# Optimization experiments

Hardware: AMD Instinct MI355X
Metric: run time of the kernel (lower is better)

Reference implementation:

```python
import jax, jax.numpy as jnp
import numpy as np

EPS = 1e-5

def _conv(x, w, b):
    # NCHW, OIHW, stride 1, SAME padding (kernel 3, padding 1)
    y = jax.lax.conv_general_dilated(x, w, (1, 1), 'SAME',
                                     dimension_numbers=('NCHW', 'OIHW', 'NCHW'))
    return y + b[None, :, None, None]

def _maxpool2(x):
    return jax.lax.reduce_window(x, -jnp.inf, jax.lax.max,
                                 (1, 1, 2, 2), (1, 1, 2, 2), 'VALID')

def _fraud_layer(v, theta, phases, sq_r, disp_r, disp_phi, kerr):
    # classical shim of a 2-mode photonic layer; all params are zero -> identity
    c, s = jnp.cos(theta), jnp.sin(theta)
    rot = jnp.array([[1.0, 0.0], [0.0, 1.0]]) * c + jnp.array([[0.0, -1.0], [1.0, 0.0]]) * s
    v = v @ rot.T
    v = v * jnp.cos(phases)          # phase shifters
    v = v * jnp.exp(sq_r)            # squeezing
    v = v + disp_r * jnp.cos(disp_phi)  # displacement
    return v + kerr * v ** 3         # Kerr nonlinearity

def setup_inputs() -> dict:
    key = jax.random.key(0)
    ks = jax.random.split(key, 16)
    B = 4096
    inp = {
        'x': jax.random.normal(ks[0], (B, 1, 32, 32), jnp.float32),
        'conv1_w': jax.random.normal(ks[1], (8, 1, 3, 3), jnp.float32) * 0.2,
        'conv1_b': jnp.zeros((8,), jnp.float32),
        'conv2_w': jax.random.normal(ks[2], (16, 8, 3, 3), jnp.float32) * 0.1,
        'conv2_b': jnp.zeros((16,), jnp.float32),
        'conv3_w': jax.random.normal(ks[3], (32, 16, 3, 3), jnp.float32) * 0.1,
        'conv3_b': jnp.zeros((32,), jnp.float32),
        'gnn_w1': jax.random.normal(ks[4], (32, 32), jnp.float32) * 0.2,
        'gnn_w2': jax.random.normal(ks[5], (16, 32), jnp.float32) * 0.2,
        'rotation_params': jax.random.normal(ks[6], (4, 4), jnp.float32),
        'entangle_params': jax.random.normal(ks[7], (3,), jnp.float32),
        'reduce_w': jax.random.normal(ks[8], (2, 32), jnp.float32) * 0.2,
        'reduce_b': jnp.zeros((2,), jnp.float32),
        'cls_w': jax.random.normal(ks[9], (2, 2), jnp.float32) * 0.5,
        'cls_b': jnp.zeros((2,), jnp.float32),
        'bn_gamma': jnp.ones((2,), jnp.float32),
        'bn_beta': jnp.zeros((2,), jnp.float32),
    }
    return inp

def reference(x, conv1_w, conv1_b, conv2_w, conv2_b, conv3_w, conv3_b,
              gnn_w1, gnn_w2, rotation_params, entangle_params,
              reduce_w, reduce_b, cls_w, cls_b, bn_gamma, bn_beta):
    B = x.shape[0]
    # CNN feature extractor
    h = jax.nn.relu(_conv(x, conv1_w, conv1_b))
    h = _maxpool2(h)
    h = jax.nn.relu(_conv(h, conv2_w, conv2_b))
    h = _maxpool2(h)
    h = jax.nn.relu(_conv(h, conv3_w, conv3_b))
    feats = jnp.mean(h, axis=(2, 3))  # AdaptiveAvgPool2d((1,1)) -> (B, 32)
    # GNN feedforward (batched equivalent of the per-sample Python loop)
    a = jnp.tanh(feats @ gnn_w1.T)    # (B, 32)
    g = jnp.tanh(a @ gnn_w2.T)        # (B, 16)
    # Quantum-style self-attention (runs on detached numpy in original -> stop_gradient)
    d = g.shape[-1]
    q = (g.reshape(B, 4, 4) @ rotation_params).reshape(B, d)
    k = (g.reshape(B, 4, 4) @ rotation_params.T).reshape(B, d)
    temp = jnp.mean(jnp.cos(entangle_params))
    logits = (q @ k.T) * (temp / jnp.sqrt(jnp.asarray(d, jnp.float32)))  # (B, B)
    attn = jax.nn.softmax(logits, axis=-1) @ g                           # (B, 16)
    rep = jnp.concatenate([g, attn], axis=-1)                            # (B, 32)
    rep = jax.lax.stop_gradient(rep)  # numpy round-trip breaks the autograd graph
    # reduce -> fraud layers (all-zero params -> identity) -> classifier
    reduced = rep @ reduce_w.T + reduce_b  # (B, 2)
    z = jnp.zeros((2,), jnp.float32)
    for _ in range(2):  # input layer + 1 hidden layer, all-zero FraudLayerParameters
        reduced = _fraud_layer(reduced, 0.0, z, z, z, z, z)
    out = reduced @ cls_w.T + cls_b  # (B, 2)
    # BatchNorm1d(2) in training mode: batch stats, biased variance
    mu = jnp.mean(out, axis=0)
    var = jnp.mean((out - mu) ** 2, axis=0)
    out = bn_gamma * (out - mu) * jax.lax.rsqrt(var + EPS) + bn_beta
    return out
```

## Files before the change

### kernel.cpp

```cpp
#include <hip/hip_runtime.h>
#include <math.h>

#define LOG2E 1.4426950408889634f

typedef _Float16 h2v __attribute__((ext_vector_type(2)));
typedef _Float16 h4  __attribute__((ext_vector_type(4)));
typedef _Float16 h8  __attribute__((ext_vector_type(8)));
typedef float    f4  __attribute__((ext_vector_type(4)));

__device__ __forceinline__ h2v pk(float a, float b) {
    return __builtin_bit_cast(h2v, __builtin_amdgcn_cvt_pkrtz(a, b));
}

__device__ __forceinline__ f4 mfma16x32(h8 a, h8 b, f4 c) {
    return __builtin_amdgcn_mfma_f32_16x16x32_f16(a, b, c, 0, 0, 0);
}

__device__ __forceinline__ f4 mfma16x16(h4 a, h4 b, f4 c) {
    return __builtin_amdgcn_mfma_f32_16x16x16f16(a, b, c, 0, 0, 0);
}

__device__ __forceinline__ float fast_tanh(float x) {
    const float xc = fminf(fmaxf(x, -15.f), 15.f);
    const float t = exp2f(xc * (2.f * LOG2E));
    return (t - 1.f) * __builtin_amdgcn_rcpf(t + 1.f);
}

__global__ __launch_bounds__(256) void k_pack(
    const float* __restrict__ w1,
    const float* __restrict__ w2, const float* __restrict__ w3,
    const float* __restrict__ ent,
    _Float16* __restrict__ w2f, _Float16* __restrict__ w3f,
    h2v* __restrict__ w1p, float* __restrict__ w1t,
    float* __restrict__ tsc)
{
    if (threadIdx.x == 0) {
        const float temp = (cosf(ent[0]) + cosf(ent[1]) + cosf(ent[2])) * (1.f / 3.f);
        tsc[0] = temp * 0.25f;
    }
    if (threadIdx.x < 24) {
        const int oc = threadIdx.x / 3, ky = threadIdx.x % 3;
        w1p[threadIdx.x] = pk(w1[oc * 9 + ky * 3 + 0], w1[oc * 9 + ky * 3 + 1]);
        w1t[threadIdx.x] = w1[oc * 9 + ky * 3 + 2];
    }
    for (int idx = threadIdx.x; idx < 1536; idx += 256) {
        const int j = idx & 7;
        const int lane = (idx >> 3) & 63;
        const int c = idx >> 9;
        const int oc = lane & 15;
        const int s = c * 4 + (lane >> 4);
        w2f[idx] = (s < 9) ? (_Float16)w2[oc * 72 + j * 9 + s] : (_Float16)0.f;
    }
    for (int idx = threadIdx.x; idx < 5120; idx += 256) {
        const int j = idx & 7;
        const int lane = (idx >> 3) & 63;
        const int rest = idx >> 9;
        const int mt = rest / 5;
        const int oc = mt * 16 + (lane & 15);
        const int kk = (lane >> 4) * 8 + j;
        const int ic = kk & 15;
        const int sh = (rest - mt * 5) * 2 + (kk >> 4);
        w3f[idx] = (sh < 9) ? (_Float16)w3[oc * 144 + ic * 9 + sh] : (_Float16)0.f;
    }
}

__global__ __launch_bounds__(256) void k_cnn(
    const float* __restrict__ x,
    const h2v* __restrict__ w1p, const float* __restrict__ w1t,
    const float* __restrict__ b1,
    const _Float16* __restrict__ w2f, const float* __restrict__ b2,
    const _Float16* __restrict__ w3f, const float* __restrict__ b3,
    const float* __restrict__ gw1,
    const float* __restrict__ gw2,
    const float* __restrict__ rot,
    const float* __restrict__ tsc,
    _Float16* __restrict__ q16, _Float16* __restrict__ k16,
    _Float16* __restrict__ g16, _Float16* __restrict__ gswz)
{
    __shared__ __align__(16) char smem[4624 + 5184 + 3200 + 256];
    float* xs   = (float*)smem;
    h8*  p1c    = (h8*)(smem + 4624);
    h8*  p2hc   = (h8*)(smem + 4624 + 5184);
    h4*  p2h4   = (h4*)(smem + 4624 + 5184);
    float* fsum = (float*)(smem + 4624 + 5184 + 3200);

    const int t = threadIdx.x;
    const int b = blockIdx.x;
    const int lane = t & 63;
    const int w = __builtin_amdgcn_readfirstlane(t >> 6);
    const int nn = lane & 15;
    const int kq = lane >> 4;

    const h8 hzero = (h8)(_Float16)0.f;
    const f4 fzero = {0.f, 0.f, 0.f, 0.f};

    const float4 v = ((const float4*)(x + (size_t)b * 1024))[t];

    if (t < 132) {
        int r, c;
        if (t < 34)       { r = 0;  c = t; }
        else if (t < 68)  { r = 33; c = t - 34; }
        else if (t < 100) { r = t - 68 + 1;  c = 0; }
        else              { r = t - 100 + 1; c = 33; }
        xs[r * 34 + c] = 0.f;
    } else if (t < 200) {
        const int u = t - 132;
        int r, c;
        if (u < 18)      { r = 0;  c = u; }
        else if (u < 36) { r = 17; c = u - 18; }
        else if (u < 52) { r = u - 36 + 1; c = 0; }
        else             { r = u - 52 + 1; c = 17; }
        p1c[r * 18 + c] = hzero;
    } else if (t < 236) {
        const int u = t - 200;
        int r, c;
        if (u < 10)      { r = 0; c = u; }
        else if (u < 20) { r = 9; c = u - 10; }
        else if (u < 28) { r = u - 20 + 1; c = 0; }
        else             { r = u - 28 + 1; c = 9; }
        p2hc[(r * 10 + c) * 2 + 0] = hzero;
        p2hc[(r * 10 + c) * 2 + 1] = hzero;
    }
    {
        const int row = t >> 3;
        const int col = (t & 7) << 2;
        float* dst = &xs[(row + 1) * 34 + col + 1];
        dst[0] = v.x; dst[1] = v.y; dst[2] = v.z; dst[3] = v.w;
    }
    __syncthreads();

    {
        const int px = t & 15, py = t >> 4;
        float pa[4][4];
        #pragma unroll
        for (int iy = 0; iy < 4; ++iy)
            #pragma unroll
            for (int ix = 0; ix < 4; ++ix)
                pa[iy][ix] = xs[(2 * py + iy) * 34 + (2 * px + ix)];
        h2v pA[4], pB[4];
        #pragma unroll
        for (int r = 0; r < 4; ++r) {
            pA[r] = pk(pa[r][0], pa[r][1]);
            pB[r] = pk(pa[r][1], pa[r][2]);
        }

        float r8[8];
        #pragma unroll
        for (int oc = 0; oc < 8; ++oc) {
            const h2v wp0 = w1p[oc * 3 + 0], wp1 = w1p[oc * 3 + 1], wp2 = w1p[oc * 3 + 2];
            const float wt0 = w1t[oc * 3 + 0], wt1 = w1t[oc * 3 + 1], wt2 = w1t[oc * 3 + 2];
            const float bb = b1[oc];
            float mx = -1e30f;
            #pragma unroll
            for (int sy = 0; sy < 2; ++sy) {
                float s0 = bb, s1 = bb;
                s0 = __builtin_amdgcn_fdot2(pA[sy],     wp0, s0, false);
                s0 = __builtin_amdgcn_fdot2(pA[sy + 1], wp1, s0, false);
                s0 = __builtin_amdgcn_fdot2(pA[sy + 2], wp2, s0, false);
                s0 = fmaf(pa[sy][2], wt0, s0);
                s0 = fmaf(pa[sy + 1][2], wt1, s0);
                s0 = fmaf(pa[sy + 2][2], wt2, s0);
                s1 = __builtin_amdgcn_fdot2(pB[sy],     wp0, s1, false);
                s1 = __builtin_amdgcn_fdot2(pB[sy + 1], wp1, s1, false);
                s1 = __builtin_amdgcn_fdot2(pB[sy + 2], wp2, s1, false);
                s1 = fmaf(pa[sy][3], wt0, s1);
                s1 = fmaf(pa[sy + 1][3], wt1, s1);
                s1 = fmaf(pa[sy + 2][3], wt2, s1);
                mx = fmaxf(mx, fmaxf(s0, s1));
            }
            r8[oc] = fmaxf(mx, 0.f);
        }
        union { h8 v; h2v p[4]; } u;
        #pragma unroll
        for (int ocp = 0; ocp < 4; ++ocp) u.p[ocp] = pk(r8[2 * ocp], r8[2 * ocp + 1]);
        p1c[(py + 1) * 18 + (px + 1)] = u.v;
    }

    h8 a2[3];
    #pragma unroll
    for (int c = 0; c < 3; ++c) a2[c] = ((const h8*)w2f)[c * 64 + lane];

    __syncthreads();

    f4 accp[4] = {fzero, fzero, fzero, fzero};
    #pragma unroll
    for (int c = 0; c < 3; ++c) {
        const int s = c * 4 + kq;
        const int ky = (s < 9) ? s / 3 : 0;
        const int kx = (s < 9) ? s % 3 : 0;
        #pragma unroll
        for (int p = 0; p < 4; ++p) {
            h8 bf = hzero;
            if (s < 9) bf = p1c[(4 * w + p + ky) * 18 + (nn + kx)];
            accp[p] = mfma16x32(a2[c], bf, accp[p]);
        }
    }

    {
        float bq[4];
        #pragma unroll
        for (int r = 0; r < 4; ++r) bq[r] = b2[kq * 4 + r];
        #pragma unroll
        for (int i = 0; i < 2; ++i) {
            float m2[4];
            #pragma unroll
            for (int r = 0; r < 4; ++r) {
                const float v0 = fmaxf(accp[2 * i][r] + bq[r], 0.f);
                const float v1 = fmaxf(accp[2 * i + 1][r] + bq[r], 0.f);
                float mv = fmaxf(v0, v1);
                mv = fmaxf(mv, __shfl_xor(mv, 1));
                m2[r] = mv;
            }
            if ((lane & 1) == 0) {
                const int px = nn >> 1;
                const int py = 2 * w + i;
                union { h4 v; h2v p[2]; } u;
                u.p[0] = pk(m2[0], m2[1]);
                u.p[1] = pk(m2[2], m2[3]);
                p2h4[((py + 1) * 10 + (px + 1)) * 4 + kq] = u.v;
            }
        }
    }

    const int mt = w >> 1;
    const int nt0 = (w & 1) * 2;
    h8 a3[5];
    #pragma unroll
    for (int c = 0; c < 5; ++c) a3[c] = ((const h8*)w3f)[(mt * 5 + c) * 64 + lane];

    __syncthreads();

    f4 acc3[2] = {fzero, fzero};
    #pragma unroll
    for (int c = 0; c < 5; ++c) {
        const int shv = 2 * c + (kq >> 1);
        const int hh = kq & 1;
        const int ky = (shv < 9) ? ((shv * 11) >> 5) : 0;
        const int kx = (shv < 9) ? (shv - 3 * ky) : 0;
        #pragma unroll
        for (int p = 0; p < 2; ++p) {
            const int pos = (nt0 + p) * 16 + nn;
            const int yy = pos >> 3, xx = pos & 7;
            h8 bf = hzero;
            if (shv < 9) bf = p2hc[((yy + ky) * 10 + (xx + kx)) * 2 + hh];
            acc3[p] = mfma16x32(a3[c], bf, acc3[p]);
        }
    }

    {
        float bq[4];
        #pragma unroll
        for (int r = 0; r < 4; ++r) bq[r] = b3[mt * 16 + kq * 4 + r];
        float sv[4];
        #pragma unroll
        for (int r = 0; r < 4; ++r) {
            float s = fmaxf(acc3[0][r] + bq[r], 0.f) + fmaxf(acc3[1][r] + bq[r], 0.f);
            #pragma unroll
            for (int off = 1; off < 16; off <<= 1) s += __shfl_xor(s, off);
            sv[r] = s;
        }
        if (nn == 0) {
            const f4 pack = {sv[0], sv[1], sv[2], sv[3]};
            ((f4*)fsum)[mt * 8 + (w & 1) * 4 + kq] = pack;
        }
    }
    __syncthreads();

    if (w != 0) return;

    const float qscale = tsc[0];

    const int l = t;
    const int i5 = l & 31;
    const float fsv = (fsum[(i5 >> 4) * 32 + (i5 & 15)] +
                       fsum[(i5 >> 4) * 32 + 16 + (i5 & 15)]) * (1.f / 64.f);

    float asv;
    {
        const int h = l >> 5;
        float s = 0.f;
        #pragma unroll
        for (int q4 = 0; q4 < 4; ++q4) {
            const float4 wv = ((const float4*)gw1)[i5 * 8 + h * 4 + q4];
            s = fmaf(wv.x, __shfl(fsv, h * 16 + q4 * 4 + 0), s);
            s = fmaf(wv.y, __shfl(fsv, h * 16 + q4 * 4 + 1), s);
            s = fmaf(wv.z, __shfl(fsv, h * 16 + q4 * 4 + 2), s);
            s = fmaf(wv.w, __shfl(fsv, h * 16 + q4 * 4 + 3), s);
        }
        s += __shfl_xor(s, 32);
        asv = fast_tanh(s);
    }

    const int i4 = l & 15;
    float gsv;
    {
        const int h = l >> 4;
        float s = 0.f;
        #pragma unroll
        for (int q4 = 0; q4 < 2; ++q4) {
            const float4 wv = ((const float4*)gw2)[i4 * 8 + h * 2 + q4];
            s = fmaf(wv.x, __shfl(asv, h * 8 + q4 * 4 + 0), s);
            s = fmaf(wv.y, __shfl(asv, h * 8 + q4 * 4 + 1), s);
            s = fmaf(wv.z, __shfl(asv, h * 8 + q4 * 4 + 2), s);
            s = fmaf(wv.w, __shfl(asv, h * 8 + q4 * 4 + 3), s);
        }
        s += __shfl_xor(s, 16);
        s += __shfl_xor(s, 32);
        gsv = fast_tanh(s);
    }

    const int grp = l >> 4;
    const int r = i4 >> 2, c = i4 & 3;
    float gq[4];
    #pragma unroll
    for (int j = 0; j < 4; ++j) gq[j] = __shfl(gsv, r * 4 + j);

    float v2;
    if (grp == 0) {
        v2 = 0.f;
        #pragma unroll
        for (int j = 0; j < 4; ++j) v2 = fmaf(gq[j], rot[j * 4 + c], v2);
        v2 *= qscale;
    } else if (grp == 1) {
        v2 = 0.f;
        #pragma unroll
        for (int j = 0; j < 4; ++j) v2 = fmaf(gq[j], rot[c * 4 + j], v2);
    } else {
        v2 = gsv;
    }
    const float vn = __shfl_xor(v2, 1);

    if (grp == 3) {
        const int tile = b >> 4, lc = b & 15;
        gswz[tile * 256 + (((lc >> 2) * 16) + i4) * 4 + (lc & 3)] = (_Float16)gsv;
    } else if ((i4 & 1) == 0) {
        const h2v pv = pk(v2, vn);
        if (grp == 0)      ((h2v*)q16)[b * 8 + (i4 >> 1)] = pv;
        else if (grp == 1) ((h2v*)k16)[b * 8 + (i4 >> 1)] = pv;
        else               ((h2v*)g16)[b * 8 + (i4 >> 1)] = pv;
    }
}

__global__ __launch_bounds__(1024) void k_attn(
    const _Float16* __restrict__ q16, const _Float16* __restrict__ k16,
    const _Float16* __restrict__ g16, const _Float16* __restrict__ gswz,
    const float* __restrict__ rw, const float* __restrict__ rb,
    const float* __restrict__ cw, const float* __restrict__ cb,
    float* __restrict__ outp, int B)
{
    __shared__ f4 lO[16][64];
    __shared__ float lm[16][16];
    __shared__ float ll[16][16];

    const int t = threadIdx.x;
    const int lane = t & 63;
    const int w = t >> 6;
    const int rt = blockIdx.x;
    const int r = lane & 15;
    const int q = lane >> 4;
    const f4 fzero = {0.f, 0.f, 0.f, 0.f};

    const h4 qf = *(const h4*)(q16 + ((size_t)(rt * 16 + r)) * 16 + q * 4);

    float m = -1e30f, lp = 0.f;
    f4 O = fzero;

    const int strip = B >> 4;
    const int cbeg = w * strip;

    h4 kf = *(const h4*)(k16 + ((size_t)(cbeg + r)) * 16 + q * 4);
    h4 gf = *(const h4*)(gswz + (size_t)(cbeg >> 4) * 256 + lane * 4);

    for (int ci = 0; ci < strip; ci += 16) {
        const int cnext = (ci + 16 < strip) ? (cbeg + ci + 16) : cbeg;
        const h4 kf_n = *(const h4*)(k16 + ((size_t)(cnext + r)) * 16 + q * 4);
        const h4 gf_n = *(const h4*)(gswz + (size_t)(cnext >> 4) * 256 + lane * 4);

        const f4 st = mfma16x16(kf, qf, fzero);

        float mx = fmaxf(fmaxf(st[0], st[1]), fmaxf(st[2], st[3]));
        mx = fmaxf(mx, __shfl_xor(mx, 16));
        mx = fmaxf(mx, __shfl_xor(mx, 32));
        if (__ballot(mx > m)) {
            const float mn = fmaxf(m, mx);
            const float a = exp2f((m - mn) * LOG2E);
            lp *= a;
            O[0] *= a; O[1] *= a; O[2] *= a; O[3] *= a;
            m = mn;
        }
        const float p0 = exp2f((st[0] - m) * LOG2E);
        const float p1 = exp2f((st[1] - m) * LOG2E);
        const float p2 = exp2f((st[2] - m) * LOG2E);
        const float p3 = exp2f((st[3] - m) * LOG2E);
        lp += (p0 + p1) + (p2 + p3);

        union { h4 v; h2v p[2]; } u;
        u.p[0] = pk(p0, p1);
        u.p[1] = pk(p2, p3);
        O = mfma16x16(gf, u.v, O);

        kf = kf_n;
        gf = gf_n;
    }
    lp += __shfl_xor(lp, 16);
    lp += __shfl_xor(lp, 32);

    lO[w][lane] = O;
    if (lane < 16) { lm[w][lane] = m; ll[w][lane] = lp; }
    __syncthreads();

    if (w == 0) {
        float M = lm[0][r];
        #pragma unroll
        for (int ww = 1; ww < 16; ++ww) M = fmaxf(M, lm[ww][r]);
        float L = 0.f;
        f4 Om = fzero;
        #pragma unroll
        for (int ww = 0; ww < 16; ++ww) {
            const float f = exp2f((lm[ww][r] - M) * LOG2E);
            L = fmaf(ll[ww][r], f, L);
            const f4 ow = lO[ww][lane];
            Om[0] = fmaf(ow[0], f, Om[0]);
            Om[1] = fmaf(ow[1], f, Om[1]);
            Om[2] = fmaf(ow[2], f, Om[2]);
            Om[3] = fmaf(ow[3], f, Om[3]);
        }
        const float il = 1.f / L;
        const h4 gr = *(const h4*)(g16 + ((size_t)(rt * 16 + r)) * 16 + q * 4);

        float rv[2];
        #pragma unroll
        for (int c = 0; c < 2; ++c) {
            float s = 0.f;
            #pragma unroll
            for (int j = 0; j < 4; ++j) {
                s = fmaf((float)gr[j], rw[c * 32 + q * 4 + j], s);
                s = fmaf(Om[j] * il, rw[c * 32 + 16 + q * 4 + j], s);
            }
            s += __shfl_xor(s, 16);
            s += __shfl_xor(s, 32);
            rv[c] = s + rb[c];
        }
        if (q == 0) {
            float2 o;
            o.x = cb[0] + cw[0] * rv[0] + cw[1] * rv[1];
            o.y = cb[1] + cw[2] * rv[0] + cw[3] * rv[1];
            ((float2*)outp)[rt * 16 + r] = o;
        }
    }
}

__global__ __launch_bounds__(1024) void k_bn(
    float* __restrict__ data, const float* __restrict__ gamma,
    const float* __restrict__ beta, int B)
{
    __shared__ float red[16][4];
    __shared__ float coef[4];
    const int t = threadIdx.x;
    float s0 = 0.f, s1 = 0.f, q0 = 0.f, q1 = 0.f;
    for (int i = t; i < B; i += 1024) {
        const float2 v = ((const float2*)data)[i];
        s0 += v.x; q0 += v.x * v.x;
        s1 += v.y; q1 += v.y * v.y;
    }
    #pragma unroll
    for (int off = 32; off; off >>= 1) {
        s0 += __shfl_xor(s0, off); q0 += __shfl_xor(q0, off);
        s1 += __shfl_xor(s1, off); q1 += __shfl_xor(q1, off);
    }
    if ((t & 63) == 0) {
        red[t >> 6][0] = s0; red[t >> 6][1] = q0;
        red[t >> 6][2] = s1; red[t >> 6][3] = q1;
    }
    __syncthreads();
    if (t == 0) {
        float S0 = 0.f, Q0 = 0.f, S1 = 0.f, Q1 = 0.f;
        for (int w = 0; w < 16; ++w) {
            S0 += red[w][0]; Q0 += red[w][1]; S1 += red[w][2]; Q1 += red[w][3];
        }
        const float inv = 1.f / (float)B;
        const float mu0 = S0 * inv, mu1 = S1 * inv;
        const float v0 = Q0 * inv - mu0 * mu0;
        const float v1 = Q1 * inv - mu1 * mu1;
        const float sc0 = gamma[0] * rsqrtf(v0 + 1e-5f);
        const float sc1 = gamma[1] * rsqrtf(v1 + 1e-5f);
        coef[0] = sc0; coef[1] = beta[0] - mu0 * sc0;
        coef[2] = sc1; coef[3] = beta[1] - mu1 * sc1;
    }
    __syncthreads();
    const float sc0 = coef[0], sh0 = coef[1], sc1 = coef[2], sh1 = coef[3];
    for (int i = t; i < B; i += 1024) {
        float2 v = ((const float2*)data)[i];
        v.x = fmaf(v.x, sc0, sh0);
        v.y = fmaf(v.y, sc1, sh1);
        ((float2*)data)[i] = v;
    }
}

extern "C" void kernel_launch(void* const* d_in, const int* in_sizes, int n_in,
                              void* d_out, int out_size, void* d_ws, size_t ws_size,
                              hipStream_t stream)
{
    (void)n_in; (void)out_size; (void)ws_size;
    const float* x   = (const float*)d_in[0];
    const float* w1  = (const float*)d_in[1];
    const float* b1  = (const float*)d_in[2];
    const float* w2  = (const float*)d_in[3];
    const float* b2  = (const float*)d_in[4];
    const float* w3  = (const float*)d_in[5];
    const float* b3  = (const float*)d_in[6];
    const float* gw1 = (const float*)d_in[7];
    const float* gw2 = (const float*)d_in[8];
    const float* rot = (const float*)d_in[9];
    const float* ent = (const float*)d_in[10];
    const float* rw  = (const float*)d_in[11];
    const float* rbv = (const float*)d_in[12];
    const float* cw  = (const float*)d_in[13];
    const float* cbv = (const float*)d_in[14];
    const float* gam = (const float*)d_in[15];
    const float* bet = (const float*)d_in[16];

    const int B = in_sizes[0] / (32 * 32);

    _Float16* q16  = (_Float16*)d_ws;
    _Float16* k16  = q16 + (size_t)B * 16;
    _Float16* g16  = k16 + (size_t)B * 16;
    _Float16* gswz = g16 + (size_t)B * 16;
    _Float16* w2f  = gswz + (size_t)B * 16;
    _Float16* w3f  = w2f + 1536;
    h2v*      w1p  = (h2v*)(w3f + 5120);
    float*    w1t  = (float*)(w1p + 24);
    float*    tsc  = w1t + 24;
    float* pre = (float*)d_out;

    k_pack<<<1, 256, 0, stream>>>(w1, w2, w3, ent, w2f, w3f, w1p, w1t, tsc);
    k_cnn<<<B, 256, 0, stream>>>(x, w1p, w1t, b1, w2f, b2, w3f, b3, gw1, gw2,
                                 rot, tsc, q16, k16, g16, gswz);
    k_attn<<<B / 16, 1024, 0, stream>>>(q16, k16, g16, gswz, rw, rbv, cw, cbv,
                                        pre, B);
    k_bn<<<1, 1024, 0, stream>>>(pre, gam, bet, B);
}
```

Before: 133.8 us.

## Use MFMA for conv1, deepen attention prefetch, fuse BN stats via atomics

Conv1 plus maxpool is recast as a 32x32x16 MFMA. A packed weight matrix covers the four pool sub-positions times eight output channels, and the 4x4 input patch is the K dimension. The attention loop prefetches two key/value tiles ahead instead of one. BatchNorm sums and squared sums are accumulated with atomics inside the attention kernel, so the BN kernel no longer rereads and reduces the whole output. In exchange, conv1 inputs are rounded to fp16, the atomic float sums are nondeterministic, and register pressure rises from the deeper prefetch.

```diff
diff --git a/kernel.cpp b/kernel.cpp
--- a/kernel.cpp
+++ b/kernel.cpp
@@ -7,6 +7,7 @@
 typedef _Float16 h4  __attribute__((ext_vector_type(4)));
 typedef _Float16 h8  __attribute__((ext_vector_type(8)));
 typedef float    f4  __attribute__((ext_vector_type(4)));
+typedef float    f16v __attribute__((ext_vector_type(16)));
 
 __device__ __forceinline__ h2v pk(float a, float b) {
     return __builtin_bit_cast(h2v, __builtin_amdgcn_cvt_pkrtz(a, b));
@@ -14,6 +15,10 @@
 
 __device__ __forceinline__ f4 mfma16x32(h8 a, h8 b, f4 c) {
     return __builtin_amdgcn_mfma_f32_16x16x32_f16(a, b, c, 0, 0, 0);
+}
+
+__device__ __forceinline__ f16v mfma32x16(h8 a, h8 b, f16v c) {
+    return __builtin_amdgcn_mfma_f32_32x32x16_f16(a, b, c, 0, 0, 0);
 }
 
 __device__ __forceinline__ f4 mfma16x16(h4 a, h4 b, f4 c) {
@@ -31,17 +36,24 @@
     const float* __restrict__ w2, const float* __restrict__ w3,
     const float* __restrict__ ent,
     _Float16* __restrict__ w2f, _Float16* __restrict__ w3f,
-    h2v* __restrict__ w1p, float* __restrict__ w1t,
-    float* __restrict__ tsc)
+    _Float16* __restrict__ w1a, float* __restrict__ tsc,
+    float* __restrict__ bnacc)
 {
     if (threadIdx.x == 0) {
         const float temp = (cosf(ent[0]) + cosf(ent[1]) + cosf(ent[2])) * (1.f / 3.f);
         tsc[0] = temp * 0.25f;
     }
-    if (threadIdx.x < 24) {
-        const int oc = threadIdx.x / 3, ky = threadIdx.x % 3;
-        w1p[threadIdx.x] = pk(w1[oc * 9 + ky * 3 + 0], w1[oc * 9 + ky * 3 + 1]);
-        w1t[threadIdx.x] = w1[oc * 9 + ky * 3 + 2];
+    if (threadIdx.x < 4) bnacc[threadIdx.x] = 0.f;
+    for (int idx = threadIdx.x; idx < 512; idx += 256) {
+        const int ln = idx >> 3, j = idx & 7;
+        const int m = ln & 31;
+        const int k = ((ln >> 5) << 3) + j;
+        const int sidx = m >> 3, oc = m & 7;
+        const int sy = sidx >> 1, sx = sidx & 1;
+        const int ry = (k >> 2) - sy, rx = (k & 3) - sx;
+        float val = 0.f;
+        if (ry >= 0 && ry < 3 && rx >= 0 && rx < 3) val = w1[oc * 9 + ry * 3 + rx];
+        w1a[idx] = (_Float16)val;
     }
     for (int idx = threadIdx.x; idx < 1536; idx += 256) {
         const int j = idx & 7;
@@ -66,7 +78,7 @@
 
 __global__ __launch_bounds__(256) void k_cnn(
     const float* __restrict__ x,
-    const h2v* __restrict__ w1p, const float* __restrict__ w1t,
+    const _Float16* __restrict__ w1a,
     const float* __restrict__ b1,
     const _Float16* __restrict__ w2f, const float* __restrict__ b2,
     const _Float16* __restrict__ w3f, const float* __restrict__ b3,
@@ -95,6 +107,8 @@
     const f4 fzero = {0.f, 0.f, 0.f, 0.f};
 
     const float4 v = ((const float4*)(x + (size_t)b * 1024))[t];
+    const h8 a1 = ((const h8*)w1a)[lane];
+    const float4 bb4 = ((const float4*)b1)[lane >> 5];
 
     if (t < 132) {
         int r, c;
@@ -130,50 +144,31 @@
     __syncthreads();
 
     {
-        const int px = t & 15, py = t >> 4;
-        float pa[4][4];
-        #pragma unroll
-        for (int iy = 0; iy < 4; ++iy)
-            #pragma unroll
-            for (int ix = 0; ix < 4; ++ix)
-                pa[iy][ix] = xs[(2 * py + iy) * 34 + (2 * px + ix)];
-        h2v pA[4], pB[4];
-        #pragma unroll
-        for (int r = 0; r < 4; ++r) {
-            pA[r] = pk(pa[r][0], pa[r][1]);
-            pB[r] = pk(pa[r][1], pa[r][2]);
-        }
-
-        float r8[8];
-        #pragma unroll
-        for (int oc = 0; oc < 8; ++oc) {
-            const h2v wp0 = w1p[oc * 3 + 0], wp1 = w1p[oc * 3 + 1], wp2 = w1p[oc * 3 + 2];
-            const float wt0 = w1t[oc * 3 + 0], wt1 = w1t[oc * 3 + 1], wt2 = w1t[oc * 3 + 2];
-            const float bb = b1[oc];
-            float mx = -1e30f;
-            #pragma unroll
-            for (int sy = 0; sy < 2; ++sy) {
-                float s0 = bb, s1 = bb;
-                s0 = __builtin_amdgcn_fdot2(pA[sy],     wp0, s0, false);
-                s0 = __builtin_amdgcn_fdot2(pA[sy + 1], wp1, s0, false);
-                s0 = __builtin_amdgcn_fdot2(pA[sy + 2], wp2, s0, false);
-                s0 = fmaf(pa[sy][2], wt0, s0);
-                s0 = fmaf(pa[sy + 1][2], wt1, s0);
-                s0 = fmaf(pa[sy + 2][2], wt2, s0);
-                s1 = __builtin_amdgcn_fdot2(pB[sy],     wp0, s1, false);
-                s1 = __builtin_amdgcn_fdot2(pB[sy + 1], wp1, s1, false);
-                s1 = __builtin_amdgcn_fdot2(pB[sy + 2], wp2, s1, false);
-                s1 = fmaf(pa[sy][3], wt0, s1);
-                s1 = fmaf(pa[sy + 1][3], wt1, s1);
-                s1 = fmaf(pa[sy + 2][3], wt2, s1);
-                mx = fmaxf(mx, fmaxf(s0, s1));
-            }
-            r8[oc] = fmaxf(mx, 0.f);
-        }
-        union { h8 v; h2v p[4]; } u;
-        #pragma unroll
-        for (int ocp = 0; ocp < 4; ++ocp) u.p[ocp] = pk(r8[2 * ocp], r8[2 * ocp + 1]);
-        p1c[(py + 1) * 18 + (px + 1)] = u.v;
+        const int n = lane & 31, h = lane >> 5;
+        const float2* xs2 = (const float2*)xs;
+        const f16v z16 = (f16v)0.f;
+        #pragma unroll
+        for (int sub = 0; sub < 2; ++sub) {
+            const int p = w * 64 + sub * 32 + n;
+            const int pyy = p >> 4, pxx = p & 15;
+            const int base = (2 * pyy + 2 * h) * 17 + pxx;
+            const float2 v00 = xs2[base],      v01 = xs2[base + 1];
+            const float2 v10 = xs2[base + 17], v11 = xs2[base + 18];
+            union { h8 v; h2v p2[4]; } bu;
+            bu.p2[0] = pk(v00.x, v00.y);
+            bu.p2[1] = pk(v01.x, v01.y);
+            bu.p2[2] = pk(v10.x, v10.y);
+            bu.p2[3] = pk(v11.x, v11.y);
+            const f16v acc = mfma32x16(a1, bu.v, z16);
+            float o0 = fmaxf(fmaxf(fmaxf(acc[0], acc[4]),  fmaxf(acc[8],  acc[12])) + bb4.x, 0.f);
+            float o1 = fmaxf(fmaxf(fmaxf(acc[1], acc[5]),  fmaxf(acc[9],  acc[13])) + bb4.y, 0.f);
+            float o2 = fmaxf(fmaxf(fmaxf(acc[2], acc[6]),  fmaxf(acc[10], acc[14])) + bb4.z, 0.f);
+            float o3 = fmaxf(fmaxf(fmaxf(acc[3], acc[7]),  fmaxf(acc[11], acc[15])) + bb4.w, 0.f);
+            union { h4 v; h2v p2[2]; } ou;
+            ou.p2[0] = pk(o0, o1);
+            ou.p2[1] = pk(o2, o3);
+            ((h4*)&p1c[(pyy + 1) * 18 + (pxx + 1)])[h] = ou.v;
+        }
     }
 
     h8 a2[3];
@@ -346,7 +341,7 @@
     const _Float16* __restrict__ g16, const _Float16* __restrict__ gswz,
     const float* __restrict__ rw, const float* __restrict__ rb,
     const float* __restrict__ cw, const float* __restrict__ cb,
-    float* __restrict__ outp, int B)
+    float* __restrict__ outp, float* __restrict__ bnacc, int B)
 {
     __shared__ f4 lO[16][64];
     __shared__ float lm[16][16];
@@ -368,15 +363,17 @@
     const int strip = B >> 4;
     const int cbeg = w * strip;
 
-    h4 kf = *(const h4*)(k16 + ((size_t)(cbeg + r)) * 16 + q * 4);
-    h4 gf = *(const h4*)(gswz + (size_t)(cbeg >> 4) * 256 + lane * 4);
+    h4 kfA = *(const h4*)(k16 + ((size_t)(cbeg + r)) * 16 + q * 4);
+    h4 gfA = *(const h4*)(gswz + (size_t)(cbeg >> 4) * 256 + lane * 4);
+    h4 kfB = *(const h4*)(k16 + ((size_t)(cbeg + 16 + r)) * 16 + q * 4);
+    h4 gfB = *(const h4*)(gswz + (size_t)((cbeg + 16) >> 4) * 256 + lane * 4);
 
     for (int ci = 0; ci < strip; ci += 16) {
-        const int cnext = (ci + 16 < strip) ? (cbeg + ci + 16) : cbeg;
-        const h4 kf_n = *(const h4*)(k16 + ((size_t)(cnext + r)) * 16 + q * 4);
-        const h4 gf_n = *(const h4*)(gswz + (size_t)(cnext >> 4) * 256 + lane * 4);
-
-        const f4 st = mfma16x16(kf, qf, fzero);
+        const int cn = (ci + 32 < strip) ? (cbeg + ci + 32) : cbeg;
+        const h4 kfC = *(const h4*)(k16 + ((size_t)(cn + r)) * 16 + q * 4);
+        const h4 gfC = *(const h4*)(gswz + (size_t)(cn >> 4) * 256 + lane * 4);
+
+        const f4 st = mfma16x16(kfA, qf, fzero);
 
         float mx = fmaxf(fmaxf(st[0], st[1]), fmaxf(st[2], st[3]));
         mx = fmaxf(mx, __shfl_xor(mx, 16));
@@ -397,10 +394,10 @@
         union { h4 v; h2v p[2]; } u;
         u.p[0] = pk(p0, p1);
         u.p[1] = pk(p2, p3);
-        O = mfma16x16(gf, u.v, O);
-
-        kf = kf_n;
-        gf = gf_n;
+        O = mfma16x16(gfA, u.v, O);
+
+        kfA = kfB; gfA = gfB;
+        kfB = kfC; gfB = gfC;
     }
     lp += __shfl_xor(lp, 16);
     lp += __shfl_xor(lp, 32);
@@ -446,42 +443,34 @@
             o.x = cb[0] + cw[0] * rv[0] + cw[1] * rv[1];
             o.y = cb[1] + cw[2] * rv[0] + cw[3] * rv[1];
             ((float2*)outp)[rt * 16 + r] = o;
+
+            float s0 = o.x, s1 = o.y, q0 = o.x * o.x, q1 = o.y * o.y;
+            #pragma unroll
+            for (int off = 1; off < 16; off <<= 1) {
+                s0 += __shfl_xor(s0, off); q0 += __shfl_xor(q0, off);
+                s1 += __shfl_xor(s1, off); q1 += __shfl_xor(q1, off);
+            }
+            if (r == 0) {
+                atomicAdd(bnacc + 0, s0);
+                atomicAdd(bnacc + 1, q0);
+                atomicAdd(bnacc + 2, s1);
+                atomicAdd(bnacc + 3, q1);
+            }
         }
     }
 }
 
 __global__ __launch_bounds__(1024) void k_bn(
-    float* __restrict__ data, const float* __restrict__ gamma,
-    const float* __restrict__ beta, int B)
+    float* __restrict__ data, const float* __restrict__ bnacc,
+    const float* __restrict__ gamma, const float* __restrict__ beta, int B)
 {
-    __shared__ float red[16][4];
     __shared__ float coef[4];
     const int t = threadIdx.x;
-    float s0 = 0.f, s1 = 0.f, q0 = 0.f, q1 = 0.f;
-    for (int i = t; i < B; i += 1024) {
-        const float2 v = ((const float2*)data)[i];
-        s0 += v.x; q0 += v.x * v.x;
-        s1 += v.y; q1 += v.y * v.y;
-    }
-    #pragma unroll
-    for (int off = 32; off; off >>= 1) {
-        s0 += __shfl_xor(s0, off); q0 += __shfl_xor(q0, off);
-        s1 += __shfl_xor(s1, off); q1 += __shfl_xor(q1, off);
-    }
-    if ((t & 63) == 0) {
-        red[t >> 6][0] = s0; red[t >> 6][1] = q0;
-        red[t >> 6][2] = s1; red[t >> 6][3] = q1;
-    }
-    __syncthreads();
     if (t == 0) {
-        float S0 = 0.f, Q0 = 0.f, S1 = 0.f, Q1 = 0.f;
-        for (int w = 0; w < 16; ++w) {
-            S0 += red[w][0]; Q0 += red[w][1]; S1 += red[w][2]; Q1 += red[w][3];
-        }
         const float inv = 1.f / (float)B;
-        const float mu0 = S0 * inv, mu1 = S1 * inv;
-        const float v0 = Q0 * inv - mu0 * mu0;
-        const float v1 = Q1 * inv - mu1 * mu1;
+        const float mu0 = bnacc[0] * inv, mu1 = bnacc[2] * inv;
+        const float v0 = bnacc[1] * inv - mu0 * mu0;
+        const float v1 = bnacc[3] * inv - mu1 * mu1;
         const float sc0 = gamma[0] * rsqrtf(v0 + 1e-5f);
         const float sc1 = gamma[1] * rsqrtf(v1 + 1e-5f);
         coef[0] = sc0; coef[1] = beta[0] - mu0 * sc0;
@@ -528,15 +517,15 @@
     _Float16* gswz = g16 + (size_t)B * 16;
     _Float16* w2f  = gswz + (size_t)B * 16;
     _Float16* w3f  = w2f + 1536;
-    h2v*      w1p  = (h2v*)(w3f + 5120);
-    float*    w1t  = (float*)(w1p + 24);
-    float*    tsc  = w1t + 24;
+    _Float16* w1a  = w3f + 5120;
+    float*    tsc  = (float*)(w1a + 512);
+    float*    bnacc = tsc + 1;
     float* pre = (float*)d_out;
 
-    k_pack<<<1, 256, 0, stream>>>(w1, w2, w3, ent, w2f, w3f, w1p, w1t, tsc);
-    k_cnn<<<B, 256, 0, stream>>>(x, w1p, w1t, b1, w2f, b2, w3f, b3, gw1, gw2,
+    k_pack<<<1, 256, 0, stream>>>(w1, w2, w3, ent, w2f, w3f, w1a, tsc, bnacc);
+    k_cnn<<<B, 256, 0, stream>>>(x, w1a, b1, w2f, b2, w3f, b3, gw1, gw2,
                                  rot, tsc, q16, k16, g16, gswz);
     k_attn<<<B / 16, 1024, 0, stream>>>(q16, k16, g16, gswz, rw, rbv, cw, cbv,
-                                        pre, B);
-    k_bn<<<1, 1024, 0, stream>>>(pre, gam, bet, B);
-}
+                                        pre, bnacc, B);
+    k_bn<<<1, 1024, 0, stream>>>(pre, bnacc, gam, bet, B);
+}
```

After: 143.2 us. +7.0%, slower.
